# Optimization experiments

Hardware: AMD Instinct MI355X
Metric: run time of the kernel (lower is better)

The kernel has to match this reference:

```python
import jax, jax.numpy as jnp
import numpy as np

N_SRC0, N_DST0, N_DST1 = 400000, 200000, 100000
E0, E1 = 3200000, 1600000
IN_FEATS, H_FEATS, NUM_CLASSES, NUM_CELL_TYPES = 128, 256, 8, 24


def setup_inputs() -> dict:
    key = jax.random.key(0)
    ks = jax.random.split(key, 12)
    feats = jax.random.normal(ks[0], (N_SRC0, IN_FEATS), dtype=jnp.float32)
    cell_ids = jax.random.randint(ks[1], (N_SRC0,), 0, NUM_CELL_TYPES)
    x = jnp.concatenate([cell_ids.astype(jnp.float32)[:, None], feats], axis=1)  # [N,129]
    src0 = jax.random.randint(ks[2], (E0,), 0, N_SRC0, dtype=jnp.int32)
    dst0 = jax.random.randint(ks[3], (E0,), 0, N_DST0, dtype=jnp.int32)
    src1 = jax.random.randint(ks[4], (E1,), 0, N_DST0, dtype=jnp.int32)
    dst1 = jax.random.randint(ks[5], (E1,), 0, N_DST1, dtype=jnp.int32)
    s = 1.0 / np.sqrt(IN_FEATS)
    s2 = 1.0 / np.sqrt(H_FEATS)
    return {
        "x": x,
        "src0": src0, "dst0": dst0, "src1": src1, "dst1": dst1,
        "n_dst0": N_DST0, "n_dst1": N_DST1,
        "emb": jax.random.normal(ks[6], (NUM_CELL_TYPES, IN_FEATS), dtype=jnp.float32),
        "W_self1": jax.random.normal(ks[7], (IN_FEATS, H_FEATS), dtype=jnp.float32) * s,
        "W_neigh1": jax.random.normal(ks[8], (IN_FEATS, H_FEATS), dtype=jnp.float32) * s,
        "b1": jnp.zeros((H_FEATS,), dtype=jnp.float32),
        "W_self2": jax.random.normal(ks[9], (H_FEATS, NUM_CLASSES), dtype=jnp.float32) * s2,
        "W_neigh2": jax.random.normal(ks[10], (H_FEATS, NUM_CLASSES), dtype=jnp.float32) * s2,
        "b2": jnp.zeros((NUM_CLASSES,), dtype=jnp.float32),
    }


def _sage_mean(h_src, h_dst, src, dst, n_dst, W_self, W_neigh, b):
    # gather src features along edges, mean-reduce onto dst nodes
    msg = h_src[src]                                                # [E, d]
    agg = jax.ops.segment_sum(msg, dst, num_segments=n_dst)        # [n_dst, d]
    deg = jax.ops.segment_sum(jnp.ones_like(dst, dtype=h_src.dtype), dst, num_segments=n_dst)
    agg = agg / jnp.maximum(deg, 1.0)[:, None]
    return h_dst @ W_self + agg @ W_neigh + b


def reference(x, src0, dst0, src1, dst1, n_dst0, n_dst1,
              emb, W_self1, W_neigh1, b1, W_self2, W_neigh2, b2):
    cell_ids = x[:, 0].astype(jnp.int32)
    feat = x[:, 1:]
    h = feat * jax.nn.sigmoid(emb[cell_ids])  # embedding-gated features; dropout = identity (eval)
    h_dst = h[:n_dst0]
    h1 = jax.nn.relu(_sage_mean(h, h_dst, src0, dst0, n_dst0, W_self1, W_neigh1, b1))
    h1_dst = h1[:n_dst1]
    out = _sage_mean(h1, h1_dst, src1, dst1, n_dst1, W_self2, W_neigh2, b2)
    return out
```

## Files before the change

### kernel.cpp

```cpp
#include <hip/hip_runtime.h>

typedef unsigned int uint;
typedef unsigned short ushort;
typedef __attribute__((ext_vector_type(8))) short short8;
typedef __attribute__((ext_vector_type(4))) float f32x4;
typedef __attribute__((ext_vector_type(2))) float f32x2;

__device__ __forceinline__ float bflo(uint u) { return __uint_as_float(u << 16); }
__device__ __forceinline__ float bfhi(uint u) { return __uint_as_float(u & 0xffff0000u); }
__device__ __forceinline__ ushort f2bf(float f) {
    uint u = __float_as_uint(f);
    u += 0x7fffu + ((u >> 16) & 1u);
    return (ushort)(u >> 16);
}
__device__ __forceinline__ uint pack2(float a, float b) {
    return (uint)f2bf(a) | ((uint)f2bf(b) << 16);
}
__device__ __forceinline__ float sigm(float e) { return 1.0f / (1.0f + __expf(-e)); }

#define ND0 200000
#define ND1 100000
#define INF 128
#define HF  256
#define BCAP 32768
#define GSTRIDE 16
#define NBKT 200
#define CAP_A 48
#define SENT 0xFFFFFFFFu

__global__ __launch_bounds__(256) void gate_k(const float* __restrict__ x,
                                              const float* __restrict__ emb,
                                              ushort* __restrict__ h, int nnodes) {
    int tid  = blockIdx.x * 256 + threadIdx.x;
    int node = tid >> 4, tq = tid & 15;
    if (node >= nnodes) return;
    const float* xr = x + (size_t)node * 129;
    int cell = (int)xr[0];
    int f0 = tq * 8;
    const float* er = emb + cell * INF + f0;
    float4 e0 = *(const float4*)er;
    float4 e1 = *(const float4*)(er + 4);
    float v[8];
    __builtin_memcpy(&v[0], xr + 1 + f0, 16);
    __builtin_memcpy(&v[4], xr + 5 + f0, 16);
    uint4 o;
    o.x = pack2(v[0] * sigm(e0.x), v[1] * sigm(e0.y));
    o.y = pack2(v[2] * sigm(e0.z), v[3] * sigm(e0.w));
    o.z = pack2(v[4] * sigm(e1.x), v[5] * sigm(e1.y));
    o.w = pack2(v[6] * sigm(e1.z), v[7] * sigm(e1.w));
    *(uint4*)(h + (size_t)node * INF + f0) = o;
}

#define SCAN_B 1024
__global__ __launch_bounds__(256) void scan1_k(const int* __restrict__ in,
                                               int* __restrict__ out,
                                               int* __restrict__ bsum, int n) {
    __shared__ int tmp[256];
    int t = threadIdx.x;
    int base = blockIdx.x * SCAN_B;
    int v[4], s = 0;
#pragma unroll
    for (int q = 0; q < 4; ++q) {
        int idx = base + t * 4 + q;
        v[q] = (idx < n) ? ((in[idx] + 7) & ~7) : 0;
        s += v[q];
    }
    tmp[t] = s; __syncthreads();
    for (int off = 1; off < 256; off <<= 1) {
        int xv = (t >= off) ? tmp[t - off] : 0; __syncthreads();
        tmp[t] += xv; __syncthreads();
    }
    int excl = tmp[t] - s;
#pragma unroll
    for (int q = 0; q < 4; ++q) {
        int idx = base + t * 4 + q;
        if (idx < n) out[idx] = excl;
        excl += v[q];
    }
    if (t == 255) bsum[blockIdx.x] = tmp[255];
}

__global__ __launch_bounds__(256) void scan2_k(int* __restrict__ bsum, int nb) {
    __shared__ int tmp[256];
    int t = threadIdx.x;
    int s = (t < nb) ? bsum[t] : 0;
    tmp[t] = s; __syncthreads();
    for (int off = 1; off < 256; off <<= 1) {
        int xv = (t >= off) ? tmp[t - off] : 0; __syncthreads();
        tmp[t] += xv; __syncthreads();
    }
    if (t < nb) bsum[t] = tmp[t] - s;
}

__global__ __launch_bounds__(256) void scan3_k(int* __restrict__ row_start,
                                               const int* __restrict__ bsum, int n) {
    int i = blockIdx.x * blockDim.x + threadIdx.x;
    if (i < n) row_start[i] += bsum[i >> 10];
}

template <int CPT>
__global__ __launch_bounds__(256) void binA_k(const int* __restrict__ src,
                                              const int* __restrict__ dst,
                                              uint* __restrict__ pairs,
                                              int* __restrict__ gcur, int E) {
    __shared__ int  lcur[NBKT];
    __shared__ uint stage[NBKT][CAP_A];
    int t = threadIdx.x;
    int c0 = blockIdx.x * (256 * CPT);
    int n = min(256 * CPT, E - c0);
    for (int i = t; i < NBKT; i += 256) lcur[i] = 0;
    __syncthreads();

    int i0 = t * CPT;
    if (i0 + CPT <= n) {
#pragma unroll
        for (int v = 0; v < CPT / 4; ++v) {
            int4 d4 = *(const int4*)(dst + c0 + i0 + v * 4);
            int4 s4 = *(const int4*)(src + c0 + i0 + v * 4);
            int dv[4] = { d4.x, d4.y, d4.z, d4.w };
            int sv[4] = { s4.x, s4.y, s4.z, s4.w };
#pragma unroll
            for (int q = 0; q < 4; ++q) {
                int d = dv[q];
                int b = d >> 10;
                uint e = ((uint)sv[q] << 10) | (uint)(d & 1023);
                int r = atomicAdd(&lcur[b], 1);
                if (r < CAP_A) stage[b][r] = e;
                else {
                    int p = atomicAdd(&gcur[b * GSTRIDE], 1);
                    pairs[(size_t)b * BCAP + p] = e;
                }
            }
        }
    } else {
        for (int q = 0; q < CPT; ++q) {
            int i = i0 + q;
            if (i >= n) break;
            int d = dst[c0 + i];
            int b = d >> 10;
            uint e = ((uint)src[c0 + i] << 10) | (uint)(d & 1023);
            int r = atomicAdd(&lcur[b], 1);
            if (r < CAP_A) stage[b][r] = e;
            else {
                int p = atomicAdd(&gcur[b * GSTRIDE], 1);
                pairs[(size_t)b * BCAP + p] = e;
            }
        }
    }
    __syncthreads();

    int wid = t >> 6, lane = t & 63;
    for (int b = wid; b < NBKT; b += 4) {
        int cnt = min(lcur[b], CAP_A);
        if (cnt == 0) continue;
        int padded = (cnt + 15) & ~15;
        int base;
        if (lane == 0) base = atomicAdd(&gcur[b * GSTRIDE], padded);
        base = __shfl(base, 0);
        if (lane < padded)
            pairs[(size_t)b * BCAP + base + lane] = (lane < cnt) ? stage[b][lane] : SENT;
    }
}

__global__ __launch_bounds__(1024) void binC_k(const uint* __restrict__ pairs,
                                               const int* __restrict__ gcur,
                                               int* __restrict__ cnt, int nd) {
    __shared__ int h[1024];
    int b = blockIdx.x, t = threadIdx.x;
    h[t] = 0;
    __syncthreads();
    int ne = gcur[b * GSTRIDE];
    const uint* bp = pairs + (size_t)b * BCAP;
    for (int i = t; i < ne; i += 1024) {
        uint e = bp[i];
        if (e != SENT) atomicAdd(&h[e & 1023], 1);
    }
    __syncthreads();
    int d = (b << 10) + t;
    if (d < nd) cnt[d] = h[t];
}

__global__ __launch_bounds__(1024) void binB_k(const uint* __restrict__ pairs,
                                               const int* __restrict__ gcur,
                                               const int* __restrict__ row_start,
                                               int* __restrict__ csr, int nd, int zrow) {
    __shared__ int cur[1024];
    int b = blockIdx.x, t = threadIdx.x;
    int dbase = b << 10;
    cur[t] = (dbase + t < nd) ? row_start[dbase + t] : 0;
    __syncthreads();
    int ne = gcur[b * GSTRIDE];
    const uint* bp = pairs + (size_t)b * BCAP;
    for (int i = t; i < ne; i += 1024) {
        uint e = bp[i];
        if (e == SENT) continue;
        int p = atomicAdd(&cur[e & 1023], 1);
        csr[p] = (int)(e >> 10);
    }
    __syncthreads();
    if (dbase + t < nd) {
        int pe = cur[t];
        int pad = (-(pe - row_start[dbase + t])) & 7;
        for (int q = 0; q < pad; ++q) csr[pe + q] = zrow;
    }
}

__global__ __launch_bounds__(256) void gather4_k(const int* __restrict__ csr,
                                                 const int* __restrict__ row_start,
                                                 const int* __restrict__ cnt,
                                                 const ushort* __restrict__ hsrc,
                                                 uint* __restrict__ aggm, int nrows) {
    int w    = (blockIdx.x * blockDim.x + threadIdx.x) >> 6;
    int lane = threadIdx.x & 63;
    if (w >= nrows) return;
    int e  = lane >> 4;
    int fo = (lane & 15) * 4;
    int beg = row_start[w], c = cnt[w];
    int end = beg + ((c + 7) & ~7);
    const uint* hb = (const uint*)hsrc;
    f32x2 A[4] = {{0.f,0.f},{0.f,0.f},{0.f,0.f},{0.f,0.f}};
    f32x2 B[4] = {{0.f,0.f},{0.f,0.f},{0.f,0.f},{0.f,0.f}};
    if (beg < end) {
        int r0 = csr[beg + e];
        int r1 = csr[beg + 4 + e];
        uint4 h0 = *(const uint4*)(hb + (size_t)r0 * 64 + fo);
        uint4 h1 = *(const uint4*)(hb + (size_t)r1 * 64 + fo);
        for (int j = beg; j < end; j += 8) {
            int n0 = 0, n1 = 0;
            if (j + 8 < end) {
                n0 = csr[j + 8 + e];
                n1 = csr[j + 12 + e];
            }
            uint4 g0 = *(const uint4*)(hb + (size_t)n0 * 64 + fo);
            uint4 g1 = *(const uint4*)(hb + (size_t)n1 * 64 + fo);
            A[0] += (f32x2){ bflo(h0.x), bfhi(h0.x) };
            A[1] += (f32x2){ bflo(h0.y), bfhi(h0.y) };
            A[2] += (f32x2){ bflo(h0.z), bfhi(h0.z) };
            A[3] += (f32x2){ bflo(h0.w), bfhi(h0.w) };
            B[0] += (f32x2){ bflo(h1.x), bfhi(h1.x) };
            B[1] += (f32x2){ bflo(h1.y), bfhi(h1.y) };
            B[2] += (f32x2){ bflo(h1.z), bfhi(h1.z) };
            B[3] += (f32x2){ bflo(h1.w), bfhi(h1.w) };
            h0 = g0; h1 = g1;
        }
    }
#pragma unroll
    for (int i = 0; i < 4; ++i) A[i] += B[i];
#pragma unroll
    for (int i = 0; i < 4; ++i) {
        A[i].x += __shfl_xor(A[i].x, 16);
        A[i].y += __shfl_xor(A[i].y, 16);
        A[i].x += __shfl_xor(A[i].x, 32);
        A[i].y += __shfl_xor(A[i].y, 32);
    }
    if (lane < 16) {
        float inv = 1.0f / fmaxf((float)c, 1.0f);
        uint4 o;
        o.x = pack2(A[0].x * inv, A[0].y * inv);
        o.y = pack2(A[1].x * inv, A[1].y * inv);
        o.z = pack2(A[2].x * inv, A[2].y * inv);
        o.w = pack2(A[3].x * inv, A[3].y * inv);
        *(uint4*)(aggm + (size_t)w * 64 + fo) = o;
    }
}

__global__ __launch_bounds__(256) void wconv_k(const float* __restrict__ Ws,
                                               const float* __restrict__ Wn,
                                               uint* __restrict__ Wb) {
    int tid  = blockIdx.x * 256 + threadIdx.x;
    int lane = tid & 63, nf = (tid >> 6) & 15, ks = tid >> 10;
    int n  = nf * 16 + (lane & 15);
    int k0 = ks * 32 + ((lane >> 4) << 3);
    uint o[4];
#pragma unroll
    for (int p = 0; p < 4; ++p) {
        int k = k0 + 2 * p;
        float a = (k < 128)     ? Ws[(size_t)k * HF + n]       : Wn[(size_t)(k - 128) * HF + n];
        float b = (k + 1 < 128) ? Ws[(size_t)(k + 1) * HF + n] : Wn[(size_t)(k - 127) * HF + n];
        o[p] = pack2(a, b);
    }
    uint4 v = { o[0], o[1], o[2], o[3] };
    *(uint4*)(Wb + (size_t)tid * 4) = v;
}

__global__ __launch_bounds__(256) void wpack2_k(const float* __restrict__ Ws2,
                                                const float* __restrict__ Wn2,
                                                uint* __restrict__ Wb2) {
    int tid = blockIdx.x * 256 + threadIdx.x;
    if (tid >= 512) return;
    int lane = tid & 63, ks = tid >> 6;
    int n  = lane & 15;
    int k0 = ks * 32 + ((lane >> 4) << 3);
    const float* W = (n < 8) ? Wn2 : Ws2;
    int c = n & 7;
    uint o[4];
#pragma unroll
    for (int p = 0; p < 4; ++p) {
        int k = k0 + 2 * p;
        o[p] = pack2(W[(size_t)k * 8 + c], W[(size_t)(k + 1) * 8 + c]);
    }
    uint4 v = { o[0], o[1], o[2], o[3] };
    *(uint4*)(Wb2 + (size_t)tid * 4) = v;
}

__global__ __launch_bounds__(256) void layer1_mfma_k(const uint* __restrict__ hb,
                                                     const uint* __restrict__ aggm,
                                                     const uint* __restrict__ Wb,
                                                     const uint* __restrict__ Wb2,
                                                     const float* __restrict__ b1,
                                                     float* __restrict__ z,
                                                     float* __restrict__ out, int nd1) {
    __shared__ uint lds[64 * 132];
    int t = threadIdx.x, lane = t & 63, wid = t >> 6;
    int quad = lane >> 4, l16 = lane & 15;
    int r0 = blockIdx.x * 64;

#pragma unroll
    for (int it = 0; it < 8; ++it) {
        int i = t + it * 256;
        int r = i >> 5, u4 = i & 31;
        const uint* src = (u4 < 16) ? (hb + (size_t)(r0 + r) * 64 + u4 * 4)
                                    : (aggm + (size_t)(r0 + r) * 64 + (u4 - 16) * 4);
        *(uint4*)&lds[r * 132 + u4 * 4] = *(const uint4*)src;
    }

    float bias[4];
#pragma unroll
    for (int i = 0; i < 4; ++i) bias[i] = b1[wid * 64 + i * 16 + l16];
    f32x4 acc[4][4];
#pragma unroll
    for (int mf = 0; mf < 4; ++mf)
#pragma unroll
        for (int i = 0; i < 4; ++i)
            acc[mf][i] = (f32x4){ bias[i], bias[i], bias[i], bias[i] };

    __syncthreads();

#pragma unroll
    for (int ks = 0; ks < 8; ++ks) {
        short8 bfr[4];
#pragma unroll
        for (int i = 0; i < 4; ++i) {
            int nf = wid * 4 + i;
            bfr[i] = *(const short8*)(Wb + (size_t)((ks * 16 + nf) * 64 + lane) * 4);
        }
        short8 afr[4];
#pragma unroll
        for (int mf = 0; mf < 4; ++mf) {
            int r = mf * 16 + l16;
            afr[mf] = *(const short8*)&lds[r * 132 + ks * 16 + quad * 4];
        }
#pragma unroll
        for (int mf = 0; mf < 4; ++mf)
#pragma unroll
            for (int i = 0; i < 4; ++i)
                acc[mf][i] = __builtin_amdgcn_mfma_f32_16x16x32_bf16(afr[mf], bfr[i],
                                                                     acc[mf][i], 0, 0, 0);
    }

    __syncthreads();
    ushort* st = (ushort*)lds;
#pragma unroll
    for (int mf = 0; mf < 4; ++mf)
#pragma unroll
        for (int i = 0; i < 4; ++i) {
            int col = wid * 64 + i * 16 + l16;
#pragma unroll
            for (int reg = 0; reg < 4; ++reg) {
                int row = mf * 16 + quad * 4 + reg;
                st[row * 264 + col] = f2bf(fmaxf(acc[mf][i][reg], 0.0f));
            }
        }
    __syncthreads();

    f32x4 zacc = (f32x4){ 0.f, 0.f, 0.f, 0.f };
    int rloc = wid * 16 + l16;
#pragma unroll
    for (int ks = 0; ks < 8; ++ks) {
        short8 a = *(const short8*)&lds[rloc * 132 + ks * 16 + quad * 4];
        short8 b = *(const short8*)(Wb2 + (size_t)(ks * 64 + lane) * 4);
        zacc = __builtin_amdgcn_mfma_f32_16x16x32_bf16(a, b, zacc, 0, 0, 0);
    }
#pragma unroll
    for (int reg = 0; reg < 4; ++reg) {
        int r = r0 + wid * 16 + quad * 4 + reg;
        if (l16 < 8) z[(size_t)r * 8 + l16] = zacc[reg];
        else if (r < nd1) out[(size_t)r * 8 + (l16 - 8)] = zacc[reg];
    }
}

__global__ __launch_bounds__(256) void gz_k(const int* __restrict__ csr,
                                            const int* __restrict__ row_start,
                                            const int* __restrict__ cnt,
                                            const float* __restrict__ z,
                                            const float* __restrict__ b2,
                                            float* __restrict__ out, int nrows) {
    int tid = blockIdx.x * 256 + threadIdx.x;
    int d = tid >> 3, c = tid & 7;
    if (d >= nrows) return;
    int beg = row_start[d], n = cnt[d];
    int end = beg + ((n + 3) & ~3);
    float a = 0.f;
    for (int j = beg; j < end; j += 4) {
        int4 s4 = *(const int4*)(csr + j);
        a += z[(size_t)s4.x * 8 + c] + z[(size_t)s4.y * 8 + c]
           + z[(size_t)s4.z * 8 + c] + z[(size_t)s4.w * 8 + c];
    }
    float inv = 1.0f / fmaxf((float)n, 1.0f);
    out[(size_t)d * 8 + c] += a * inv + b2[c];
}

extern "C" void kernel_launch(void* const* d_in, const int* in_sizes, int n_in,
                              void* d_out, int out_size, void* d_ws, size_t ws_size,
                              hipStream_t stream) {
    const float* x    = (const float*)d_in[0];
    const int*   src0 = (const int*)d_in[1];
    const int*   dst0 = (const int*)d_in[2];
    const int*   src1 = (const int*)d_in[3];
    const int*   dst1 = (const int*)d_in[4];
    const float* emb  = (const float*)d_in[7];
    const float* Ws1  = (const float*)d_in[8];
    const float* Wn1  = (const float*)d_in[9];
    const float* b1   = (const float*)d_in[10];
    const float* Ws2  = (const float*)d_in[11];
    const float* Wn2  = (const float*)d_in[12];
    const float* b2   = (const float*)d_in[13];
    int E0 = in_sizes[1];
    int E1 = in_sizes[3];
    int nsrc = in_sizes[0] / 129;

    char* p = (char*)d_ws;
    ushort* h         = (ushort*)p;  p += ((size_t)nsrc + 1) * INF * 2;
    uint*   aggm      = (uint*)p;    p += (size_t)ND0 * 64 * 4;
    int*    csr       = (int*)p;     p += ((size_t)E0 + 7 * (size_t)ND0 + 16) * 4;
    int*    cnt       = (int*)p;     p += (size_t)ND0 * 4;
    int*    row_start = (int*)p;     p += (size_t)ND0 * 4;
    int*    bsum      = (int*)p;     p += 256 * 4;
    int*    gcur      = (int*)p;     p += 256 * GSTRIDE * 4;
    uint*   Wb        = (uint*)p;    p += 8192 * 16;
    uint*   Wb2       = (uint*)p;    p += 512 * 16;
    float*  z         = (float*)p;   p += ((size_t)ND0 + 1) * 8 * 4;
    uint*   pairs     = aggm;

    int ZR0 = nsrc;
    int ZR1 = ND0;

    hipMemsetAsync(gcur, 0, 256 * GSTRIDE * 4, stream);
    hipMemsetAsync(h + (size_t)ZR0 * INF, 0, INF * 2, stream);
    gate_k<<<(nsrc * 16 + 255) / 256, 256, 0, stream>>>(x, emb, h, nsrc);
    wconv_k<<<32, 256, 0, stream>>>(Ws1, Wn1, Wb);
    wpack2_k<<<2, 256, 0, stream>>>(Ws2, Wn2, Wb2);
    int nb0 = (ND0 + SCAN_B - 1) / SCAN_B;
    int ch0 = (E0 + 256 * 16 - 1) / (256 * 16);
    binA_k<16><<<ch0, 256, 0, stream>>>(src0, dst0, pairs, gcur, E0);
    binC_k<<<nb0, 1024, 0, stream>>>(pairs, gcur, cnt, ND0);
    scan1_k<<<nb0, 256, 0, stream>>>(cnt, row_start, bsum, ND0);
    scan2_k<<<1, 256, 0, stream>>>(bsum, nb0);
    scan3_k<<<(ND0 + 255) / 256, 256, 0, stream>>>(row_start, bsum, ND0);
    binB_k<<<nb0, 1024, 0, stream>>>(pairs, gcur, row_start, csr, ND0, ZR0);
    gather4_k<<<(ND0 + 3) / 4, 256, 0, stream>>>(csr, row_start, cnt, h, aggm, ND0);
    layer1_mfma_k<<<ND0 / 64, 256, 0, stream>>>((const uint*)h, aggm, Wb, Wb2, b1,
                                                z, (float*)d_out, ND1);

    hipMemsetAsync(gcur, 0, 256 * GSTRIDE * 4, stream);
    hipMemsetAsync(z + (size_t)ZR1 * 8, 0, 8 * 4, stream);
    int nb1 = (ND1 + SCAN_B - 1) / SCAN_B;
    int ch1 = (E1 + 256 * 8 - 1) / (256 * 8);
    binA_k<8><<<ch1, 256, 0, stream>>>(src1, dst1, pairs, gcur, E1);
    binC_k<<<nb1, 1024, 0, stream>>>(pairs, gcur, cnt, ND1);
    scan1_k<<<nb1, 256, 0, stream>>>(cnt, row_start, bsum, ND1);
    scan2_k<<<1, 256, 0, stream>>>(bsum, nb1);
    scan3_k<<<(ND1 + 255) / 256, 256, 0, stream>>>(row_start, bsum, ND1);
    binB_k<<<nb1, 1024, 0, stream>>>(pairs, gcur, row_start, csr, ND1, ZR1);
    gz_k<<<(ND1 * 8 + 255) / 256, 256, 0, stream>>>(csr, row_start, cnt, z, b2,
                                                    (float*)d_out, ND1);
}
```

Baseline: 724.1 us.

## Fuse per-bucket scan into histogram kernel and drop scan passes

Moves the intra-bucket exclusive scan into binC_k so the histogram and local prefix are computed in one kernel. Consumers add the block offset from bsum on the fly, which removes scan1_k and scan3_k. binB_k now resets gcur, so the second memset can go. The gather loop's software prefetch of the next feature rows is also removed: only the next indices are preloaded and row loads happen inside the loop. That cuts register use but exposes more load latency.

After: 712.9 us. Within noise of the previous version (-1.6%).

```diff
diff --git a/kernel.cpp b/kernel.cpp
--- a/kernel.cpp
+++ b/kernel.cpp
@@ -51,35 +51,6 @@
     *(uint4*)(h + (size_t)node * INF + f0) = o;
 }
 
-#define SCAN_B 1024
-__global__ __launch_bounds__(256) void scan1_k(const int* __restrict__ in,
-                                               int* __restrict__ out,
-                                               int* __restrict__ bsum, int n) {
-    __shared__ int tmp[256];
-    int t = threadIdx.x;
-    int base = blockIdx.x * SCAN_B;
-    int v[4], s = 0;
-#pragma unroll
-    for (int q = 0; q < 4; ++q) {
-        int idx = base + t * 4 + q;
-        v[q] = (idx < n) ? ((in[idx] + 7) & ~7) : 0;
-        s += v[q];
-    }
-    tmp[t] = s; __syncthreads();
-    for (int off = 1; off < 256; off <<= 1) {
-        int xv = (t >= off) ? tmp[t - off] : 0; __syncthreads();
-        tmp[t] += xv; __syncthreads();
-    }
-    int excl = tmp[t] - s;
-#pragma unroll
-    for (int q = 0; q < 4; ++q) {
-        int idx = base + t * 4 + q;
-        if (idx < n) out[idx] = excl;
-        excl += v[q];
-    }
-    if (t == 255) bsum[blockIdx.x] = tmp[255];
-}
-
 __global__ __launch_bounds__(256) void scan2_k(int* __restrict__ bsum, int nb) {
     __shared__ int tmp[256];
     int t = threadIdx.x;
@@ -90,12 +61,6 @@
         tmp[t] += xv; __syncthreads();
     }
     if (t < nb) bsum[t] = tmp[t] - s;
-}
-
-__global__ __launch_bounds__(256) void scan3_k(int* __restrict__ row_start,
-                                               const int* __restrict__ bsum, int n) {
-    int i = blockIdx.x * blockDim.x + threadIdx.x;
-    if (i < n) row_start[i] += bsum[i >> 10];
 }
 
 template <int CPT>
@@ -164,30 +129,47 @@
 
 __global__ __launch_bounds__(1024) void binC_k(const uint* __restrict__ pairs,
                                                const int* __restrict__ gcur,
-                                               int* __restrict__ cnt, int nd) {
-    __shared__ int h[1024];
+                                               int* __restrict__ cnt,
+                                               int* __restrict__ row_start,
+                                               int* __restrict__ bsum, int nd) {
+    __shared__ int hh[1024];
+    __shared__ int sc[1024];
     int b = blockIdx.x, t = threadIdx.x;
-    h[t] = 0;
+    hh[t] = 0;
     __syncthreads();
     int ne = gcur[b * GSTRIDE];
     const uint* bp = pairs + (size_t)b * BCAP;
     for (int i = t; i < ne; i += 1024) {
         uint e = bp[i];
-        if (e != SENT) atomicAdd(&h[e & 1023], 1);
-    }
-    __syncthreads();
+        if (e != SENT) atomicAdd(&hh[e & 1023], 1);
+    }
+    __syncthreads();
+    int hv = hh[t];
+    int v  = (hv + 7) & ~7;
+    sc[t] = v;
+    __syncthreads();
+    for (int off = 1; off < 1024; off <<= 1) {
+        int xv = (t >= off) ? sc[t - off] : 0; __syncthreads();
+        sc[t] += xv; __syncthreads();
+    }
     int d = (b << 10) + t;
-    if (d < nd) cnt[d] = h[t];
+    if (d < nd) {
+        cnt[d]       = hv;
+        row_start[d] = sc[t] - v;
+    }
+    if (t == 1023) bsum[b] = sc[1023];
 }
 
 __global__ __launch_bounds__(1024) void binB_k(const uint* __restrict__ pairs,
-                                               const int* __restrict__ gcur,
+                                               int* __restrict__ gcur,
                                                const int* __restrict__ row_start,
+                                               const int* __restrict__ bsum,
                                                int* __restrict__ csr, int nd, int zrow) {
     __shared__ int cur[1024];
     int b = blockIdx.x, t = threadIdx.x;
     int dbase = b << 10;
-    cur[t] = (dbase + t < nd) ? row_start[dbase + t] : 0;
+    int gbase = bsum[b];
+    cur[t] = (dbase + t < nd) ? gbase + row_start[dbase + t] : 0;
     __syncthreads();
     int ne = gcur[b * GSTRIDE];
     const uint* bp = pairs + (size_t)b * BCAP;
@@ -200,13 +182,16 @@
     __syncthreads();
     if (dbase + t < nd) {
         int pe = cur[t];
-        int pad = (-(pe - row_start[dbase + t])) & 7;
+        int st = gbase + row_start[dbase + t];
+        int pad = (-(pe - st)) & 7;
         for (int q = 0; q < pad; ++q) csr[pe + q] = zrow;
     }
+    if (t == 0) gcur[b * GSTRIDE] = 0;
 }
 
 __global__ __launch_bounds__(256) void gather4_k(const int* __restrict__ csr,
                                                  const int* __restrict__ row_start,
+                                                 const int* __restrict__ bsum,
                                                  const int* __restrict__ cnt,
                                                  const ushort* __restrict__ hsrc,
                                                  uint* __restrict__ aggm, int nrows) {
@@ -215,7 +200,7 @@
     if (w >= nrows) return;
     int e  = lane >> 4;
     int fo = (lane & 15) * 4;
-    int beg = row_start[w], c = cnt[w];
+    int beg = bsum[w >> 10] + row_start[w], c = cnt[w];
     int end = beg + ((c + 7) & ~7);
     const uint* hb = (const uint*)hsrc;
     f32x2 A[4] = {{0.f,0.f},{0.f,0.f},{0.f,0.f},{0.f,0.f}};
@@ -223,16 +208,14 @@
     if (beg < end) {
         int r0 = csr[beg + e];
         int r1 = csr[beg + 4 + e];
-        uint4 h0 = *(const uint4*)(hb + (size_t)r0 * 64 + fo);
-        uint4 h1 = *(const uint4*)(hb + (size_t)r1 * 64 + fo);
         for (int j = beg; j < end; j += 8) {
             int n0 = 0, n1 = 0;
             if (j + 8 < end) {
                 n0 = csr[j + 8 + e];
                 n1 = csr[j + 12 + e];
             }
-            uint4 g0 = *(const uint4*)(hb + (size_t)n0 * 64 + fo);
-            uint4 g1 = *(const uint4*)(hb + (size_t)n1 * 64 + fo);
+            uint4 h0 = *(const uint4*)(hb + (size_t)r0 * 64 + fo);
+            uint4 h1 = *(const uint4*)(hb + (size_t)r1 * 64 + fo);
             A[0] += (f32x2){ bflo(h0.x), bfhi(h0.x) };
             A[1] += (f32x2){ bflo(h0.y), bfhi(h0.y) };
             A[2] += (f32x2){ bflo(h0.z), bfhi(h0.z) };
@@ -241,7 +224,7 @@
             B[1] += (f32x2){ bflo(h1.y), bfhi(h1.y) };
             B[2] += (f32x2){ bflo(h1.z), bfhi(h1.z) };
             B[3] += (f32x2){ bflo(h1.w), bfhi(h1.w) };
-            h0 = g0; h1 = g1;
+            r0 = n0; r1 = n1;
         }
     }
 #pragma unroll
@@ -391,6 +374,7 @@
 
 __global__ __launch_bounds__(256) void gz_k(const int* __restrict__ csr,
                                             const int* __restrict__ row_start,
+                                            const int* __restrict__ bsum,
                                             const int* __restrict__ cnt,
                                             const float* __restrict__ z,
                                             const float* __restrict__ b2,
@@ -398,7 +382,7 @@
     int tid = blockIdx.x * 256 + threadIdx.x;
     int d = tid >> 3, c = tid & 7;
     if (d >= nrows) return;
-    int beg = row_start[d], n = cnt[d];
+    int beg = bsum[d >> 10] + row_start[d], n = cnt[d];
     int end = beg + ((n + 3) & ~3);
     float a = 0.f;
     for (int j = beg; j < end; j += 4) {
@@ -450,28 +434,23 @@
     gate_k<<<(nsrc * 16 + 255) / 256, 256, 0, stream>>>(x, emb, h, nsrc);
     wconv_k<<<32, 256, 0, stream>>>(Ws1, Wn1, Wb);
     wpack2_k<<<2, 256, 0, stream>>>(Ws2, Wn2, Wb2);
-    int nb0 = (ND0 + SCAN_B - 1) / SCAN_B;
+    int nb0 = (ND0 + 1023) / 1024;
     int ch0 = (E0 + 256 * 16 - 1) / (256 * 16);
     binA_k<16><<<ch0, 256, 0, stream>>>(src0, dst0, pairs, gcur, E0);
-    binC_k<<<nb0, 1024, 0, stream>>>(pairs, gcur, cnt, ND0);
-    scan1_k<<<nb0, 256, 0, stream>>>(cnt, row_start, bsum, ND0);
+    binC_k<<<nb0, 1024, 0, stream>>>(pairs, gcur, cnt, row_start, bsum, ND0);
     scan2_k<<<1, 256, 0, stream>>>(bsum, nb0);
-    scan3_k<<<(ND0 + 255) / 256, 256, 0, stream>>>(row_start, bsum, ND0);
-    binB_k<<<nb0, 1024, 0, stream>>>(pairs, gcur, row_start, csr, ND0, ZR0);
-    gather4_k<<<(ND0 + 3) / 4, 256, 0, stream>>>(csr, row_start, cnt, h, aggm, ND0);
+    binB_k<<<nb0, 1024, 0, stream>>>(pairs, gcur, row_start, bsum, csr, ND0, ZR0);
+    gather4_k<<<(ND0 + 3) / 4, 256, 0, stream>>>(csr, row_start, bsum, cnt, h, aggm, ND0);
     layer1_mfma_k<<<ND0 / 64, 256, 0, stream>>>((const uint*)h, aggm, Wb, Wb2, b1,
                                                 z, (float*)d_out, ND1);
 
-    hipMemsetAsync(gcur, 0, 256 * GSTRIDE * 4, stream);
     hipMemsetAsync(z + (size_t)ZR1 * 8, 0, 8 * 4, stream);
-    int nb1 = (ND1 + SCAN_B - 1) / SCAN_B;
+    int nb1 = (ND1 + 1023) / 1024;
     int ch1 = (E1 + 256 * 8 - 1) / (256 * 8);
     binA_k<8><<<ch1, 256, 0, stream>>>(src1, dst1, pairs, gcur, E1);
-    binC_k<<<nb1, 1024, 0, stream>>>(pairs, gcur, cnt, ND1);
-    scan1_k<<<nb1, 256, 0, stream>>>(cnt, row_start, bsum, ND1);
+    binC_k<<<nb1, 1024, 0, stream>>>(pairs, gcur, cnt, row_start, bsum, ND1);
     scan2_k<<<1, 256, 0, stream>>>(bsum, nb1);
-    scan3_k<<<(ND1 + 255) / 256, 256, 0, stream>>>(row_start, bsum, ND1);
-    binB_k<<<nb1, 1024, 0, stream>>>(pairs, gcur, row_start, csr, ND1, ZR1);
-    gz_k<<<(ND1 * 8 + 255) / 256, 256, 0, stream>>>(csr, row_start, cnt, z, b2,
+    binB_k<<<nb1, 1024, 0, stream>>>(pairs, gcur, row_start, bsum, csr, ND1, ZR1);
+    gz_k<<<(ND1 * 8 + 255) / 256, 256, 0, stream>>>(csr, row_start, bsum, cnt, z, b2,
                                                     (float*)d_out, ND1);
 }
```
